# Kernel optimization log

Measured on AMD Instinct MI355X. Metric: run time of the kernel, lower is better.

The kernel has to match this reference:

```python
import jax, jax.numpy as jnp
import numpy as np

N, E = 50000, 800000
IN, HID, OUT, EH = 128, 64, 128, 32  # node dims, edge-MLP hidden=32
N_ETYPES, N_NTYPES = 3, 2


def setup_inputs() -> dict:
    key = jax.random.key(0)
    ks = jax.random.split(key, 12)
    w = lambda k, shape, fan: jax.random.normal(k, shape, jnp.float32) / np.float32(np.sqrt(fan))
    nf = jax.random.normal(ks[0], (N, IN), jnp.float32)
    edge_index = jax.random.randint(ks[1], (2, E), 0, N, dtype=jnp.int32)
    edge_type = jax.random.randint(ks[2], (E,), 0, N_ETYPES, dtype=jnp.int32)
    node_type = jax.random.randint(ks[3], (N,), 0, N_NTYPES, dtype=jnp.int32)
    return {
        "nf": nf,
        "edge_index": edge_index,
        "edge_type": edge_type,
        "node_type": node_type,
        # layer 0: 128 -> 64
        "eW0": w(ks[4], (N_ETYPES, 2 * IN, EH), 2 * IN),
        "eb0": jax.random.normal(ks[5], (N_ETYPES, EH), jnp.float32) * 0.01,
        "nW0": w(ks[6], (N_NTYPES, N_ETYPES * EH, HID), N_ETYPES * EH),
        "nb0": jax.random.normal(ks[7], (N_NTYPES, HID), jnp.float32) * 0.01,
        # layer 1: 64 -> 128
        "eW1": w(ks[8], (N_ETYPES, 2 * HID, EH), 2 * HID),
        "eb1": jax.random.normal(ks[9], (N_ETYPES, EH), jnp.float32) * 0.01,
        "nW1": w(ks[10], (N_NTYPES, N_ETYPES * EH, OUT), N_ETYPES * EH),
        "nb1": jax.random.normal(ks[11], (N_NTYPES, OUT), jnp.float32) * 0.01,
    }


def _layer(nf, eW, eb, nW, nb, src, dst, edge_type, node_type):
    """One GraphNeuralNetLayer: per-edge-type message MLP + mean-scatter, then per-node-type update MLP."""
    n = nf.shape[0]
    # edge gather + concat: [E, 2*in]
    feat = jnp.concatenate([nf[src], nf[dst]], axis=-1)
    msgs = []
    for e in range(eW.shape[0]):  # fixed, small number of edge types
        m = jax.nn.relu(feat @ eW[e] + eb[e])            # [E, EH]
        mask = (edge_type == e).astype(nf.dtype)          # select this edge type
        s = jax.ops.segment_sum(m * mask[:, None], dst, num_segments=n)
        cnt = jax.ops.segment_sum(mask, dst, num_segments=n)
        # mean over mailbox; nodes with no type-e in-edges get zeros
        msgs.append(s / jnp.maximum(cnt, 1.0)[:, None])
    h = jnp.concatenate(msgs, axis=-1)                    # [N, 3*EH]
    out0 = jax.nn.relu(h @ nW[0] + nb[0])
    out1 = jax.nn.relu(h @ nW[1] + nb[1])
    return jnp.where((node_type == 0)[:, None], out0, out1)


def reference(nf, edge_index, edge_type, node_type, eW0, eb0, nW0, nb0, eW1, eb1, nW1, nb1):
    src, dst = edge_index[0], edge_index[1]
    h = _layer(nf, eW0, eb0, nW0, nb0, src, dst, edge_type, node_type)   # [N, 64]
    return _layer(h, eW1, eb1, nW1, nb1, src, dst, edge_type, node_type) # [N, 128]
```

## Files before the change

kernel.cpp:

```cpp
#include <hip/hip_runtime.h>


typedef __attribute__((ext_vector_type(8))) short bf16x8_t;
typedef __attribute__((ext_vector_type(4))) float f32x4_t;

__device__ __forceinline__ void cvt_split(float x, unsigned short& h, unsigned short& l) {
  unsigned u = __float_as_uint(x);
  unsigned rh = u + 0x7FFFu + ((u >> 16) & 1u);
  h = (unsigned short)(rh >> 16);
  float xh = __uint_as_float((unsigned)h << 16);
  float xl = x - xh;
  unsigned v = __float_as_uint(xl);
  unsigned rl = v + 0x7FFFu + ((v >> 16) & 1u);
  l = (unsigned short)(rl >> 16);
}


__global__ __launch_bounds__(256) void rank_kernel(const int* __restrict__ dst,
                                                   int* __restrict__ deg8,
                                                   int* __restrict__ rank, int E) {
  int i = blockIdx.x * 256 + threadIdx.x;
  if (i < E) {
    int d = dst[i];
    int r = (i >> 8) & 7;
    rank[i] = atomicAdd(&deg8[d * 8 + r], 1);
  }
}

__global__ __launch_bounds__(256) void scan1_kernel(int* __restrict__ deg8,
                                                    int* __restrict__ rowstart,
                                                    int* __restrict__ bsum, int n) {
  __shared__ int tmp[256];
  int t = threadIdx.x;
  int base = blockIdx.x * 1024 + t * 4;
  int vdeg[4];
#pragma unroll
  for (int q = 0; q < 4; ++q) {
    int v = base + q;
    int d = 0;
    if (v < n) {
      int4 a = *(int4*)(deg8 + (size_t)v * 8);
      int4 b = *(int4*)(deg8 + (size_t)v * 8 + 4);
      int p1 = a.x, p2 = p1 + a.y, p3 = p2 + a.z, p4 = p3 + a.w;
      int p5 = p4 + b.x, p6 = p5 + b.y, p7 = p6 + b.z;
      d = p7 + b.w;
      *(int4*)(deg8 + (size_t)v * 8) = make_int4(0, p1, p2, p3);
      *(int4*)(deg8 + (size_t)v * 8 + 4) = make_int4(p4, p5, p6, p7);
    }
    vdeg[q] = d;
  }
  int s = vdeg[0] + vdeg[1] + vdeg[2] + vdeg[3];
  tmp[t] = s;
  __syncthreads();
  for (int off = 1; off < 256; off <<= 1) {
    int u = (t >= off) ? tmp[t - off] : 0;
    __syncthreads();
    tmp[t] += u;
    __syncthreads();
  }
  int excl = tmp[t] - s;
  if (base < n)     rowstart[base]     = excl;
  if (base + 1 < n) rowstart[base + 1] = excl + vdeg[0];
  if (base + 2 < n) rowstart[base + 2] = excl + vdeg[0] + vdeg[1];
  if (base + 3 < n) rowstart[base + 3] = excl + vdeg[0] + vdeg[1] + vdeg[2];
  if (t == 255) bsum[blockIdx.x] = tmp[255];
}

__global__ __launch_bounds__(64) void scan2_kernel(const int* __restrict__ bsum,
                                                   int* __restrict__ boff, int nb,
                                                   int* __restrict__ rowstart, int n,
                                                   int* __restrict__ tcnt) {
  int lane = threadIdx.x;
  if (lane < 2) tcnt[lane] = 0;
  int v = (lane < nb) ? bsum[lane] : 0;
  int incl = v;
  for (int off = 1; off < 64; off <<= 1) {
    int u = __shfl_up(incl, off, 64);
    if (lane >= off) incl += u;
  }
  if (lane < nb) boff[lane] = incl - v;
  if (lane == 63) rowstart[n] = incl;
}

__global__ __launch_bounds__(256) void fill_kernel(const int* __restrict__ src,
                                                   const int* __restrict__ dst,
                                                   const int* __restrict__ etype,
                                                   const int* __restrict__ rank,
                                                   const int* __restrict__ rowstart,
                                                   const int* __restrict__ boff,
                                                   const int* __restrict__ deg8,
                                                   int* __restrict__ edata, int E) {
  int i = blockIdx.x * 256 + threadIdx.x;
  if (i < E) {
    int d = dst[i];
    int r = (i >> 8) & 7;
    int et = etype[i];
    int pos = rowstart[d] + boff[d >> 10] + deg8[d * 8 + r] + rank[i];
    edata[pos] = src[i] * 768 + et * 129;
  }
}


__global__ __launch_bounds__(256) void partition_kernel(const int* __restrict__ ntype,
                                                        int* __restrict__ idxbuf,
                                                        int* __restrict__ tcnt,
                                                        int n, int ncap) {
  int i = blockIdx.x * 256 + threadIdx.x;
  int lane = threadIdx.x & 63;
  int t = (i < n) ? ntype[i] : -1;
  unsigned long long m0 = __ballot(t == 0);
  unsigned long long m1 = __ballot(t == 1);
  int b0 = 0, b1 = 0;
  if (lane == 0) {
    b0 = atomicAdd(&tcnt[0], (int)__popcll(m0));
    b1 = atomicAdd(&tcnt[1], (int)__popcll(m1));
  }
  b0 = __shfl(b0, 0);
  b1 = __shfl(b1, 0);
  unsigned long long below = (1ull << lane) - 1ull;
  if (t == 0) idxbuf[b0 + (int)__popcll(m0 & below)] = i;
  else if (t == 1) idxbuf[ncap + b1 + (int)__popcll(m1 & below)] = i;
}


template <int IN, int OUT>
__global__ __launch_bounds__(256) void prep_w(const float* __restrict__ eW,
                                              float* __restrict__ wfh,
                                              float* __restrict__ wfl,
                                              const float* __restrict__ nW,
                                              float* __restrict__ wnh,
                                              float* __restrict__ wnl,
                                              int* __restrict__ zbuf, int zn4) {
  constexpr int KC = IN / 32;
  constexpr int CT = OUT / 16;
  int id = blockIdx.x * 256 + threadIdx.x;
  if (zbuf) {
    int4* zb = (int4*)zbuf;
    int tot = gridDim.x * 256;
    for (int z = id; z < zn4; z += tot) zb[z] = make_int4(0, 0, 0, 0);
  }
  if (id < 12 * KC * 64) {
    int lane = id & 63;
    int fk = id >> 6;
    int kc = fk % KC, ct = fk / KC;
    int n = ct * 16 + (lane & 15);
    int kb = kc * 32 + ((lane >> 4) & 3) * 8;
    int half = (n >= 96) ? 1 : 0;
    int jj = n - 96 * half;
    int e = jj >> 5, o = jj & 31;
    const float* wp = eW + ((size_t)((e * 2 + half) * IN) + kb) * 32 + o;
    bf16x8_t hv, lv;
#pragma unroll
    for (int j = 0; j < 8; ++j) {
      unsigned short h, l;
      cvt_split(wp[(size_t)j * 32], h, l);
      hv[j] = (short)h;
      lv[j] = (short)l;
    }
    *(bf16x8_t*)(wfh + (size_t)id * 4) = hv;
    *(bf16x8_t*)(wfl + (size_t)id * 4) = lv;
    return;
  }
  int id2 = id - 12 * KC * 64;
  if (id2 >= 2 * CT * 3 * 64) return;
  int lane = id2 & 63;
  int fk = id2 >> 6;
  int kc = fk % 3;
  int ct = (fk / 3) % CT;
  int t = fk / (3 * CT);
  const float* wp = nW + ((size_t)t * 96 + kc * 32 + ((lane >> 4) & 3) * 8) * OUT +
                    ct * 16 + (lane & 15);
  bf16x8_t hv, lv;
#pragma unroll
  for (int j = 0; j < 8; ++j) {
    unsigned short h, l;
    cvt_split(wp[(size_t)j * OUT], h, l);
    hv[j] = (short)h;
    lv[j] = (short)l;
  }
  *(bf16x8_t*)(wnh + (size_t)id2 * 4) = hv;
  *(bf16x8_t*)(wnl + (size_t)id2 * 4) = lv;
}


template <int IN>
__global__ __launch_bounds__(256) void proj_mfma(const float* __restrict__ X,
                                                 const float* __restrict__ wfh,
                                                 const float* __restrict__ wfl,
                                                 float* __restrict__ P, int n) {
  constexpr int KC = IN / 32;
  __shared__ short Ah[4 * KC * 64 * 8];
  __shared__ short Al[4 * KC * 64 * 8];
  const int tx = threadIdx.x;
  const int base = blockIdx.x * 64;

  for (int q = tx; q < 4 * KC * 64; q += 256) {
    int lane = q & 63;
    int fk = q >> 6;
    int kc = fk % KC, nt = fk / KC;
    int node = base + nt * 16 + (lane & 15);
    int kb = kc * 32 + ((lane >> 4) & 3) * 8;
    float xs[8];
    if (node < n) {
      float4 a = *(const float4*)(X + (size_t)node * IN + kb);
      float4 b = *(const float4*)(X + (size_t)node * IN + kb + 4);
      xs[0] = a.x; xs[1] = a.y; xs[2] = a.z; xs[3] = a.w;
      xs[4] = b.x; xs[5] = b.y; xs[6] = b.z; xs[7] = b.w;
    } else {
#pragma unroll
      for (int j = 0; j < 8; ++j) xs[j] = 0.f;
    }
    bf16x8_t hv, lv;
#pragma unroll
    for (int j = 0; j < 8; ++j) {
      unsigned short h, l;
      cvt_split(xs[j], h, l);
      hv[j] = (short)h;
      lv[j] = (short)l;
    }
    *(bf16x8_t*)(Ah + (size_t)q * 8) = hv;
    *(bf16x8_t*)(Al + (size_t)q * 8) = lv;
  }
  __syncthreads();

  const int wave = tx >> 6;
  const int lane = tx & 63;

  f32x4_t acc[4][3];
#pragma unroll
  for (int nt = 0; nt < 4; ++nt)
#pragma unroll
    for (int c = 0; c < 3; ++c) acc[nt][c] = (f32x4_t){0.f, 0.f, 0.f, 0.f};

  for (int kc = 0; kc < KC; ++kc) {
    bf16x8_t Bh[3], Bl[3];
#pragma unroll
    for (int c = 0; c < 3; ++c) {
      int ct = wave * 3 + c;
      size_t idx = ((size_t)(ct * KC + kc) * 64 + lane) * 4;
      Bh[c] = *(const bf16x8_t*)(wfh + idx);
      Bl[c] = *(const bf16x8_t*)(wfl + idx);
    }
#pragma unroll
    for (int nt = 0; nt < 4; ++nt) {
      size_t idx = ((size_t)(nt * KC + kc) * 64 + lane) * 8;
      bf16x8_t ah = *(const bf16x8_t*)(Ah + idx);
      bf16x8_t al = *(const bf16x8_t*)(Al + idx);
#pragma unroll
      for (int c = 0; c < 3; ++c) {
        acc[nt][c] = __builtin_amdgcn_mfma_f32_16x16x32_bf16(ah, Bh[c], acc[nt][c], 0, 0, 0);
        acc[nt][c] = __builtin_amdgcn_mfma_f32_16x16x32_bf16(ah, Bl[c], acc[nt][c], 0, 0, 0);
        acc[nt][c] = __builtin_amdgcn_mfma_f32_16x16x32_bf16(al, Bh[c], acc[nt][c], 0, 0, 0);
      }
    }
  }

  const int row0 = ((lane >> 4) & 3) * 4;
  const int col = lane & 15;
#pragma unroll
  for (int nt = 0; nt < 4; ++nt) {
#pragma unroll
    for (int c = 0; c < 3; ++c) {
      int jcol = (wave * 3 + c) * 16 + col;
#pragma unroll
      for (int r = 0; r < 4; ++r) {
        int node = base + nt * 16 + row0 + r;
        if (node < n) P[(size_t)node * 192 + jcol] = acc[nt][c][r];
      }
    }
  }
}


#define ACC_EDGE4(pk, v)                                              \
  {                                                                   \
    int et_ = (pk) & 3;                                               \
    float4 pb_ = (et_ == 0) ? pdb0 : ((et_ == 1) ? pdb1 : pdb2);      \
    float mx_ = fmaxf((v).x + pb_.x, 0.f);                            \
    float my_ = fmaxf((v).y + pb_.y, 0.f);                            \
    float mz_ = fmaxf((v).z + pb_.z, 0.f);                            \
    float mw_ = fmaxf((v).w + pb_.w, 0.f);                            \
    bool e0_ = (et_ == 0), e1_ = (et_ == 1), e2_ = (et_ == 2);        \
    a0.x += e0_ ? mx_ : 0.f; a0.y += e0_ ? my_ : 0.f;                 \
    a0.z += e0_ ? mz_ : 0.f; a0.w += e0_ ? mw_ : 0.f;                 \
    a1.x += e1_ ? mx_ : 0.f; a1.y += e1_ ? my_ : 0.f;                 \
    a1.z += e1_ ? mz_ : 0.f; a1.w += e1_ ? mw_ : 0.f;                 \
    a2.x += e2_ ? mx_ : 0.f; a2.y += e2_ ? my_ : 0.f;                 \
    a2.z += e2_ ? mz_ : 0.f; a2.w += e2_ ? mw_ : 0.f;                 \
    c0 += e0_; c1 += e1_;                                             \
  }

__global__ __launch_bounds__(256) void aggregate_kernel(const float* __restrict__ P,
                                                        const int* __restrict__ rowstart,
                                                        const int* __restrict__ boff,
                                                        const int* __restrict__ edata,
                                                        const float* __restrict__ eb,
                                                        float* __restrict__ h, int n) {
  int wid = (blockIdx.x * 256 + threadIdx.x) >> 6;
  if (wid >= n) return;
  int lane = threadIdx.x & 63;
  int co = (lane & 7) * 4;
  int cb = co * 4;
  int slot = lane >> 3;
  const float* Pd = P + (size_t)wid * 192 + 96;
  float4 pdb0 = *(const float4*)(Pd + co);
  float4 pdb1 = *(const float4*)(Pd + 32 + co);
  float4 pdb2 = *(const float4*)(Pd + 64 + co);
  float4 ebv;
  ebv = *(const float4*)(eb + co);
  pdb0.x += ebv.x; pdb0.y += ebv.y; pdb0.z += ebv.z; pdb0.w += ebv.w;
  ebv = *(const float4*)(eb + 32 + co);
  pdb1.x += ebv.x; pdb1.y += ebv.y; pdb1.z += ebv.z; pdb1.w += ebv.w;
  ebv = *(const float4*)(eb + 64 + co);
  pdb2.x += ebv.x; pdb2.y += ebv.y; pdb2.z += ebv.z; pdb2.w += ebv.w;

  int s = rowstart[wid] + boff[wid >> 10];
  int e = rowstart[wid + 1] + ((wid + 1 < n) ? boff[(wid + 1) >> 10] : 0);
  const char* Pb = (const char*)P;
  float4 a0 = make_float4(0.f, 0.f, 0.f, 0.f);
  float4 a1 = a0, a2 = a0;
  int c0 = 0, c1 = 0;
  int i = s + slot;
  for (; i + 8 < e; i += 16) {
    int p0 = edata[i];
    int p1 = edata[i + 8];
    float4 v0 = *(const float4*)(Pb + (size_t)(p0 & ~3) + cb);
    float4 v1 = *(const float4*)(Pb + (size_t)(p1 & ~3) + cb);
    ACC_EDGE4(p0, v0)
    ACC_EDGE4(p1, v1)
  }
  for (; i < e; i += 8) {
    int pk = edata[i];
    float4 v = *(const float4*)(Pb + (size_t)(pk & ~3) + cb);
    ACC_EDGE4(pk, v)
  }
#pragma unroll
  for (int off = 8; off < 64; off <<= 1) {
    a0.x += __shfl_xor(a0.x, off); a0.y += __shfl_xor(a0.y, off);
    a0.z += __shfl_xor(a0.z, off); a0.w += __shfl_xor(a0.w, off);
    a1.x += __shfl_xor(a1.x, off); a1.y += __shfl_xor(a1.y, off);
    a1.z += __shfl_xor(a1.z, off); a1.w += __shfl_xor(a1.w, off);
    a2.x += __shfl_xor(a2.x, off); a2.y += __shfl_xor(a2.y, off);
    a2.z += __shfl_xor(a2.z, off); a2.w += __shfl_xor(a2.w, off);
    c0 += __shfl_xor(c0, off);
    c1 += __shfl_xor(c1, off);
  }
  if (slot == 0) {
    int total = e - s;
    float d0 = fmaxf((float)c0, 1.f);
    float d1 = fmaxf((float)c1, 1.f);
    float d2 = fmaxf((float)(total - c0 - c1), 1.f);
    float* hn = h + (size_t)wid * 96;
    *(float4*)(hn + co)      = make_float4(a0.x / d0, a0.y / d0, a0.z / d0, a0.w / d0);
    *(float4*)(hn + 32 + co) = make_float4(a1.x / d1, a1.y / d1, a1.z / d1, a1.w / d1);
    *(float4*)(hn + 64 + co) = make_float4(a2.x / d2, a2.y / d2, a2.z / d2, a2.w / d2);
  }
}


template <int OUT>
__global__ __launch_bounds__(256) void mlp2_mfma(const float* __restrict__ H,
                                                 const float* __restrict__ wnh,
                                                 const float* __restrict__ wnl,
                                                 const float* __restrict__ nb,
                                                 const int* __restrict__ idxbuf,
                                                 const int* __restrict__ tcnt,
                                                 float* __restrict__ out, int ncap) {
  constexpr int CT = OUT / 16;
  constexpr int CW = CT / 4;
  __shared__ short Ah[12 * 64 * 8];
  __shared__ short Al[12 * 64 * 8];

  int c0 = tcnt[0];
  int nb0 = (c0 + 63) >> 6;
  int t, base, cnt;
  if ((int)blockIdx.x < nb0) {
    t = 0; base = blockIdx.x << 6; cnt = c0;
  } else {
    t = 1; base = ((int)blockIdx.x - nb0) << 6; cnt = tcnt[1];
    if (base >= cnt) return;
  }
  const int* il = idxbuf + (size_t)t * ncap;
  const float* bias = nb + t * OUT;

  const int tx = threadIdx.x;
  for (int q = tx; q < 12 * 64; q += 256) {
    int lane = q & 63;
    int fk = q >> 6;
    int kc = fk % 3, mt = fk / 3;
    int slot = base + mt * 16 + (lane & 15);
    int kb = kc * 32 + ((lane >> 4) & 3) * 8;
    float xs[8];
    if (slot < cnt) {
      int row = il[slot];
      float4 a = *(const float4*)(H + (size_t)row * 96 + kb);
      float4 b = *(const float4*)(H + (size_t)row * 96 + kb + 4);
      xs[0] = a.x; xs[1] = a.y; xs[2] = a.z; xs[3] = a.w;
      xs[4] = b.x; xs[5] = b.y; xs[6] = b.z; xs[7] = b.w;
    } else {
#pragma unroll
      for (int j = 0; j < 8; ++j) xs[j] = 0.f;
    }
    bf16x8_t hv, lv;
#pragma unroll
    for (int j = 0; j < 8; ++j) {
      unsigned short h, l;
      cvt_split(xs[j], h, l);
      hv[j] = (short)h;
      lv[j] = (short)l;
    }
    *(bf16x8_t*)(Ah + (size_t)q * 8) = hv;
    *(bf16x8_t*)(Al + (size_t)q * 8) = lv;
  }
  __syncthreads();

  const int wave = tx >> 6;
  const int lane = tx & 63;

  f32x4_t acc[4][CW];
#pragma unroll
  for (int mt = 0; mt < 4; ++mt)
#pragma unroll
    for (int c = 0; c < CW; ++c) acc[mt][c] = (f32x4_t){0.f, 0.f, 0.f, 0.f};

  for (int kc = 0; kc < 3; ++kc) {
    bf16x8_t Bh[CW], Bl[CW];
#pragma unroll
    for (int c = 0; c < CW; ++c) {
      int ct = wave * CW + c;
      size_t idx = ((size_t)((t * CT + ct) * 3 + kc) * 64 + lane) * 4;
      Bh[c] = *(const bf16x8_t*)(wnh + idx);
      Bl[c] = *(const bf16x8_t*)(wnl + idx);
    }
#pragma unroll
    for (int mt = 0; mt < 4; ++mt) {
      size_t idx = ((size_t)((mt * 3 + kc) * 64) + lane) * 8;
      bf16x8_t ah = *(const bf16x8_t*)(Ah + idx);
      bf16x8_t al = *(const bf16x8_t*)(Al + idx);
#pragma unroll
      for (int c = 0; c < CW; ++c) {
        acc[mt][c] = __builtin_amdgcn_mfma_f32_16x16x32_bf16(ah, Bh[c], acc[mt][c], 0, 0, 0);
        acc[mt][c] = __builtin_amdgcn_mfma_f32_16x16x32_bf16(ah, Bl[c], acc[mt][c], 0, 0, 0);
        acc[mt][c] = __builtin_amdgcn_mfma_f32_16x16x32_bf16(al, Bh[c], acc[mt][c], 0, 0, 0);
      }
    }
  }

  const int row0 = ((lane >> 4) & 3) * 4;
  const int col = lane & 15;
#pragma unroll
  for (int mt = 0; mt < 4; ++mt) {
#pragma unroll
    for (int c = 0; c < CW; ++c) {
      int jcol = (wave * CW + c) * 16 + col;
      float bj = bias[jcol];
#pragma unroll
      for (int r = 0; r < 4; ++r) {
        int slot = base + mt * 16 + row0 + r;
        if (slot < cnt) {
          int row = il[slot];
          out[(size_t)row * OUT + jcol] = fmaxf(acc[mt][c][r] + bj, 0.f);
        }
      }
    }
  }
}


extern "C" void kernel_launch(void* const* d_in, const int* in_sizes, int n_in,
                              void* d_out, int out_size, void* d_ws, size_t ws_size,
                              hipStream_t stream) {
  const float* nf    = (const float*)d_in[0];
  const int*   eidx  = (const int*)d_in[1];
  const int*   etype = (const int*)d_in[2];
  const int*   ntype = (const int*)d_in[3];
  const float* eW0   = (const float*)d_in[4];
  const float* eb0   = (const float*)d_in[5];
  const float* nW0   = (const float*)d_in[6];
  const float* nb0   = (const float*)d_in[7];
  const float* eW1   = (const float*)d_in[8];
  const float* eb1   = (const float*)d_in[9];
  const float* nW1   = (const float*)d_in[10];
  const float* nb1   = (const float*)d_in[11];
  const int N = in_sizes[3];
  const int E = in_sizes[2];
  const int* srcv = eidx;
  const int* dstv = eidx + E;

  float* P   = (float*)d_ws;
  float* h96 = P + (size_t)N * 192;
  float* h64 = h96 + (size_t)N * 96;
  int* rowstart = (int*)(h64 + (size_t)N * 64);
  int* tcnt     = rowstart + ((N + 4) & ~3);
  int* bsum     = tcnt + 2;
  int* boff     = bsum + 64;
  int* idxbuf   = boff + 64;
  int* edata    = idxbuf + 2 * N;
  float* wf0h   = (float*)(edata + E);
  float* wf0l   = wf0h + 12288;
  float* wf1h   = wf0l + 12288;
  float* wf1l   = wf1h + 6144;
  float* wn0h   = wf1l + 6144;
  float* wn0l   = wn0h + 6144;
  float* wn1h   = wn0l + 6144;
  float* wn1l   = wn1h + 12288;
  int* rank     = (int*)h96;
  int* deg8     = (int*)h64;

  const int nsb = (N + 1023) / 1024;
  const int egrid = (E + 255) / 256;

  prep_w<128, 128><<<24, 256, 0, stream>>>(eW0, wf0h, wf0l, nW1, wn1h, wn1l, deg8, N * 2);
  prep_w<64, 64><<<12, 256, 0, stream>>>(eW1, wf1h, wf1l, nW0, wn0h, wn0l, nullptr, 0);
  rank_kernel<<<egrid, 256, 0, stream>>>(dstv, deg8, rank, E);
  scan1_kernel<<<nsb, 256, 0, stream>>>(deg8, rowstart, bsum, N);
  scan2_kernel<<<1, 64, 0, stream>>>(bsum, boff, nsb, rowstart, N, tcnt);
  partition_kernel<<<(N + 255) / 256, 256, 0, stream>>>(ntype, idxbuf, tcnt, N, N);
  fill_kernel<<<egrid, 256, 0, stream>>>(srcv, dstv, etype, rank, rowstart, boff, deg8, edata, E);

  const int pgrid = (N + 63) / 64;
  int agrid = (N + 3) / 4;
  int mgrid = (N + 63) / 64 + 2;

  proj_mfma<128><<<pgrid, 256, 0, stream>>>(nf, wf0h, wf0l, P, N);
  aggregate_kernel<<<agrid, 256, 0, stream>>>(P, rowstart, boff, edata, eb0, h96, N);
  mlp2_mfma<64><<<mgrid, 256, 0, stream>>>(h96, wn0h, wn0l, nb0, idxbuf, tcnt, h64, N);

  proj_mfma<64><<<pgrid, 256, 0, stream>>>(h64, wf1h, wf1l, P, N);
  aggregate_kernel<<<agrid, 256, 0, stream>>>(P, rowstart, boff, edata, eb1, h96, N);
  mlp2_mfma<128><<<mgrid, 256, 0, stream>>>(h96, wn1h, wn1l, nb1, idxbuf, tcnt, (float*)d_out, N);
}
```

Baseline: 296.3 us.

## Store projected edge features and aggregated messages in fp16

Switches the per-node projection buffer P and the aggregated message buffer h from fp32 to fp16, halving the bytes gathered per edge in the aggregate kernel. The aggregate kernel is reorganised so each lane loads 8 halves (16 bytes) per edge with 16 edge slots per wave, and the packed edge offsets are rescaled to match the smaller row stride. This targets gather bandwidth in the edge aggregation, at the cost of fp16 rounding on intermediate features, which may affect accuracy tolerance.

```diff
diff --git a/kernel.cpp b/kernel.cpp
--- a/kernel.cpp
+++ b/kernel.cpp
@@ -3,6 +3,8 @@
 
 typedef __attribute__((ext_vector_type(8))) short bf16x8_t;
 typedef __attribute__((ext_vector_type(4))) float f32x4_t;
+typedef _Float16 f16;
+typedef __attribute__((ext_vector_type(8))) _Float16 f16x8_t;
 
 __device__ __forceinline__ void cvt_split(float x, unsigned short& h, unsigned short& l) {
   unsigned u = __float_as_uint(x);
@@ -96,7 +98,7 @@
     int r = (i >> 8) & 7;
     int et = etype[i];
     int pos = rowstart[d] + boff[d >> 10] + deg8[d * 8 + r] + rank[i];
-    edata[pos] = src[i] * 768 + et * 129;
+    edata[pos] = src[i] * 384 + et * 65;
   }
 }
 
@@ -187,7 +189,7 @@
 __global__ __launch_bounds__(256) void proj_mfma(const float* __restrict__ X,
                                                  const float* __restrict__ wfh,
                                                  const float* __restrict__ wfl,
-                                                 float* __restrict__ P, int n) {
+                                                 f16* __restrict__ P, int n) {
   constexpr int KC = IN / 32;
   __shared__ short Ah[4 * KC * 64 * 8];
   __shared__ short Al[4 * KC * 64 * 8];
@@ -265,83 +267,85 @@
 #pragma unroll
       for (int r = 0; r < 4; ++r) {
         int node = base + nt * 16 + row0 + r;
-        if (node < n) P[(size_t)node * 192 + jcol] = acc[nt][c][r];
+        if (node < n) P[(size_t)node * 192 + jcol] = (f16)acc[nt][c][r];
       }
     }
   }
 }
 
 
-#define ACC_EDGE4(pk, v)                                              \
-  {                                                                   \
-    int et_ = (pk) & 3;                                               \
-    float4 pb_ = (et_ == 0) ? pdb0 : ((et_ == 1) ? pdb1 : pdb2);      \
-    float mx_ = fmaxf((v).x + pb_.x, 0.f);                            \
-    float my_ = fmaxf((v).y + pb_.y, 0.f);                            \
-    float mz_ = fmaxf((v).z + pb_.z, 0.f);                            \
-    float mw_ = fmaxf((v).w + pb_.w, 0.f);                            \
-    bool e0_ = (et_ == 0), e1_ = (et_ == 1), e2_ = (et_ == 2);        \
-    a0.x += e0_ ? mx_ : 0.f; a0.y += e0_ ? my_ : 0.f;                 \
-    a0.z += e0_ ? mz_ : 0.f; a0.w += e0_ ? mw_ : 0.f;                 \
-    a1.x += e1_ ? mx_ : 0.f; a1.y += e1_ ? my_ : 0.f;                 \
-    a1.z += e1_ ? mz_ : 0.f; a1.w += e1_ ? mw_ : 0.f;                 \
-    a2.x += e2_ ? mx_ : 0.f; a2.y += e2_ ? my_ : 0.f;                 \
-    a2.z += e2_ ? mz_ : 0.f; a2.w += e2_ ? mw_ : 0.f;                 \
-    c0 += e0_; c1 += e1_;                                             \
-  }
-
-__global__ __launch_bounds__(256) void aggregate_kernel(const float* __restrict__ P,
+__global__ __launch_bounds__(256) void aggregate_kernel(const f16* __restrict__ P,
                                                         const int* __restrict__ rowstart,
                                                         const int* __restrict__ boff,
                                                         const int* __restrict__ edata,
                                                         const float* __restrict__ eb,
-                                                        float* __restrict__ h, int n) {
+                                                        f16* __restrict__ h, int n) {
   int wid = (blockIdx.x * 256 + threadIdx.x) >> 6;
   if (wid >= n) return;
   int lane = threadIdx.x & 63;
-  int co = (lane & 7) * 4;
-  int cb = co * 4;
-  int slot = lane >> 3;
-  const float* Pd = P + (size_t)wid * 192 + 96;
-  float4 pdb0 = *(const float4*)(Pd + co);
-  float4 pdb1 = *(const float4*)(Pd + 32 + co);
-  float4 pdb2 = *(const float4*)(Pd + 64 + co);
-  float4 ebv;
-  ebv = *(const float4*)(eb + co);
-  pdb0.x += ebv.x; pdb0.y += ebv.y; pdb0.z += ebv.z; pdb0.w += ebv.w;
-  ebv = *(const float4*)(eb + 32 + co);
-  pdb1.x += ebv.x; pdb1.y += ebv.y; pdb1.z += ebv.z; pdb1.w += ebv.w;
-  ebv = *(const float4*)(eb + 64 + co);
-  pdb2.x += ebv.x; pdb2.y += ebv.y; pdb2.z += ebv.z; pdb2.w += ebv.w;
-
+  int cg = lane & 3;
+  int cb = cg * 16;
+  int slot = lane >> 2;
+  const f16* Pd = P + (size_t)wid * 192 + 96;
+  float pdb0[8], pdb1[8], pdb2[8];
+  {
+    f16x8_t d0 = *(const f16x8_t*)(Pd + cg * 8);
+    f16x8_t d1 = *(const f16x8_t*)(Pd + 32 + cg * 8);
+    f16x8_t d2 = *(const f16x8_t*)(Pd + 64 + cg * 8);
+#pragma unroll
+    for (int j = 0; j < 8; ++j) {
+      pdb0[j] = (float)d0[j] + eb[cg * 8 + j];
+      pdb1[j] = (float)d1[j] + eb[32 + cg * 8 + j];
+      pdb2[j] = (float)d2[j] + eb[64 + cg * 8 + j];
+    }
+  }
   int s = rowstart[wid] + boff[wid >> 10];
   int e = rowstart[wid + 1] + ((wid + 1 < n) ? boff[(wid + 1) >> 10] : 0);
   const char* Pb = (const char*)P;
-  float4 a0 = make_float4(0.f, 0.f, 0.f, 0.f);
-  float4 a1 = a0, a2 = a0;
+  float a0[8], a1[8], a2[8];
+#pragma unroll
+  for (int j = 0; j < 8; ++j) { a0[j] = 0.f; a1[j] = 0.f; a2[j] = 0.f; }
   int c0 = 0, c1 = 0;
   int i = s + slot;
-  for (; i + 8 < e; i += 16) {
+
+#define ACC_EDGE8(pk, v)                                            \
+  {                                                                 \
+    int et_ = (pk) & 3;                                             \
+    bool e0_ = (et_ == 0), e1_ = (et_ == 1), e2_ = (et_ == 2);      \
+    _Pragma("unroll")                                               \
+    for (int j = 0; j < 8; ++j) {                                   \
+      float pb_ = e0_ ? pdb0[j] : (e1_ ? pdb1[j] : pdb2[j]);        \
+      float m_ = fmaxf((float)(v)[j] + pb_, 0.f);                   \
+      a0[j] += e0_ ? m_ : 0.f;                                      \
+      a1[j] += e1_ ? m_ : 0.f;                                      \
+      a2[j] += e2_ ? m_ : 0.f;                                      \
+    }                                                               \
+    c0 += e0_; c1 += e1_;                                           \
+  }
+
+  for (; i + 16 < e; i += 32) {
     int p0 = edata[i];
-    int p1 = edata[i + 8];
-    float4 v0 = *(const float4*)(Pb + (size_t)(p0 & ~3) + cb);
-    float4 v1 = *(const float4*)(Pb + (size_t)(p1 & ~3) + cb);
-    ACC_EDGE4(p0, v0)
-    ACC_EDGE4(p1, v1)
-  }
-  for (; i < e; i += 8) {
+    int p1 = edata[i + 16];
+    f16x8_t v0 = *(const f16x8_t*)(Pb + (size_t)(p0 & ~3) + cb);
+    f16x8_t v1 = *(const f16x8_t*)(Pb + (size_t)(p1 & ~3) + cb);
+    ACC_EDGE8(p0, v0)
+    ACC_EDGE8(p1, v1)
+  }
+  for (; i < e; i += 16) {
     int pk = edata[i];
-    float4 v = *(const float4*)(Pb + (size_t)(pk & ~3) + cb);
-    ACC_EDGE4(pk, v)
-  }
-#pragma unroll
-  for (int off = 8; off < 64; off <<= 1) {
-    a0.x += __shfl_xor(a0.x, off); a0.y += __shfl_xor(a0.y, off);
-    a0.z += __shfl_xor(a0.z, off); a0.w += __shfl_xor(a0.w, off);
-    a1.x += __shfl_xor(a1.x, off); a1.y += __shfl_xor(a1.y, off);
-    a1.z += __shfl_xor(a1.z, off); a1.w += __shfl_xor(a1.w, off);
-    a2.x += __shfl_xor(a2.x, off); a2.y += __shfl_xor(a2.y, off);
-    a2.z += __shfl_xor(a2.z, off); a2.w += __shfl_xor(a2.w, off);
+    f16x8_t v = *(const f16x8_t*)(Pb + (size_t)(pk & ~3) + cb);
+    ACC_EDGE8(pk, v)
+  }
+#undef ACC_EDGE8
+
+#pragma unroll
+  for (int off = 4; off < 64; off <<= 1) {
+#pragma unroll
+    for (int j = 0; j < 8; ++j) {
+      a0[j] += __shfl_xor(a0[j], off);
+      a1[j] += __shfl_xor(a1[j], off);
+      a2[j] += __shfl_xor(a2[j], off);
+    }
     c0 += __shfl_xor(c0, off);
     c1 += __shfl_xor(c1, off);
   }
@@ -350,16 +354,23 @@
     float d0 = fmaxf((float)c0, 1.f);
     float d1 = fmaxf((float)c1, 1.f);
     float d2 = fmaxf((float)(total - c0 - c1), 1.f);
-    float* hn = h + (size_t)wid * 96;
-    *(float4*)(hn + co)      = make_float4(a0.x / d0, a0.y / d0, a0.z / d0, a0.w / d0);
-    *(float4*)(hn + 32 + co) = make_float4(a1.x / d1, a1.y / d1, a1.z / d1, a1.w / d1);
-    *(float4*)(hn + 64 + co) = make_float4(a2.x / d2, a2.y / d2, a2.z / d2, a2.w / d2);
+    f16* hn = h + (size_t)wid * 96 + cg * 8;
+    f16x8_t o0, o1, o2;
+#pragma unroll
+    for (int j = 0; j < 8; ++j) {
+      o0[j] = (f16)(a0[j] / d0);
+      o1[j] = (f16)(a1[j] / d1);
+      o2[j] = (f16)(a2[j] / d2);
+    }
+    *(f16x8_t*)(hn)      = o0;
+    *(f16x8_t*)(hn + 32) = o1;
+    *(f16x8_t*)(hn + 64) = o2;
   }
 }
 
 
 template <int OUT>
-__global__ __launch_bounds__(256) void mlp2_mfma(const float* __restrict__ H,
+__global__ __launch_bounds__(256) void mlp2_mfma(const f16* __restrict__ H,
                                                  const float* __restrict__ wnh,
                                                  const float* __restrict__ wnl,
                                                  const float* __restrict__ nb,
@@ -393,10 +404,9 @@
     float xs[8];
     if (slot < cnt) {
       int row = il[slot];
-      float4 a = *(const float4*)(H + (size_t)row * 96 + kb);
-      float4 b = *(const float4*)(H + (size_t)row * 96 + kb + 4);
-      xs[0] = a.x; xs[1] = a.y; xs[2] = a.z; xs[3] = a.w;
-      xs[4] = b.x; xs[5] = b.y; xs[6] = b.z; xs[7] = b.w;
+      f16x8_t a = *(const f16x8_t*)(H + (size_t)row * 96 + kb);
+#pragma unroll
+      for (int j = 0; j < 8; ++j) xs[j] = (float)a[j];
     } else {
 #pragma unroll
       for (int j = 0; j < 8; ++j) xs[j] = 0.f;
@@ -487,9 +497,10 @@
   const int* srcv = eidx;
   const int* dstv = eidx + E;
 
-  float* P   = (float*)d_ws;
-  float* h96 = P + (size_t)N * 192;
-  float* h64 = h96 + (size_t)N * 96;
+  float* ws  = (float*)d_ws;
+  f16*   P   = (f16*)ws;
+  f16*   h96 = (f16*)(ws + (size_t)N * 192);
+  float* h64 = ws + (size_t)N * 192 + (size_t)N * 96;
   int* rowstart = (int*)(h64 + (size_t)N * 64);
   int* tcnt     = rowstart + ((N + 4) & ~3);
   int* bsum     = tcnt + 2;
@@ -504,7 +515,7 @@
   float* wn0l   = wn0h + 6144;
   float* wn1h   = wn0l + 6144;
   float* wn1l   = wn1h + 12288;
-  int* rank     = (int*)h96;
+  int* rank     = (int*)(ws + (size_t)N * 192);
   int* deg8     = (int*)h64;
 
   const int nsb = (N + 1023) / 1024;
```

Result: slower. 359.5 us (+21.3%).
